# Optimization experiments

Measured on AMD Instinct MI355X. Metric: run time of the kernel, lower is better.

## Reference

```python
import jax, jax.numpy as jnp
import numpy as np

N = 50000      # nodes
E = 800000     # edges (before self-loops)
H = 8          # attention heads
C = 16         # hidden per head (n_hid)
CH = H * C     # 128 = concat channel width
L = 3          # n_layer
F_IN = 128     # n_feat
N_CLASS = 40
NEG_SLOPE = 0.2


def setup_inputs() -> dict:
    key = jax.random.key(0)
    ks = jax.random.split(key, 14)
    s = 0.1
    return {
        "x": jax.random.normal(ks[0], (N, F_IN), jnp.float32),
        "edge_index": jax.random.randint(ks[1], (2, E), 0, N, jnp.int32),
        # layer 0: in F_IN -> H heads of C
        "W0":   jax.random.normal(ks[2], (F_IN, H * C), jnp.float32) * s,
        "as0":  jax.random.normal(ks[3], (H, C), jnp.float32) * s,
        "ad0":  jax.random.normal(ks[4], (H, C), jnp.float32) * s,
        "b0":   jnp.zeros((H * C,), jnp.float32),
        # layers 1..L-1 (stacked): in CH -> H heads of C
        "W12":  jax.random.normal(ks[5], (L - 1, CH, H * C), jnp.float32) * s,
        "as12": jax.random.normal(ks[6], (L - 1, H, C), jnp.float32) * s,
        "ad12": jax.random.normal(ks[7], (L - 1, H, C), jnp.float32) * s,
        "b12":  jnp.zeros((L - 1, H * C), jnp.float32),
        # attention-based skip aggregation over layers
        "Watt": jax.random.normal(ks[8], (CH, CH), jnp.float32) * s,
        "aatt": jax.random.normal(ks[9], (CH,), jnp.float32) * s,
        # output head
        "Wout": jax.random.normal(ks[10], (CH, N_CLASS), jnp.float32) * s,
        "bout": jnp.zeros((N_CLASS,), jnp.float32),
    }


def _gat_layer(x, W, a_src, a_dst, b, src, dst):
    # x: [N, F]; W: [F, H*C]; a_src/a_dst: [H, C]; b: [H*C]
    h = (x @ W).reshape(N, H, C)                                 # [N,H,C]
    s_src = jnp.einsum("nhc,hc->nh", h, a_src)                   # [N,H]
    s_dst = jnp.einsum("nhc,hc->nh", h, a_dst)                   # [N,H]
    e = jax.nn.leaky_relu(s_src[src] + s_dst[dst], NEG_SLOPE)    # [Et,H]
    # segment softmax over incoming edges of each dst node
    e_max = jax.ops.segment_max(e, dst, num_segments=N)          # [N,H]
    ee = jnp.exp(e - e_max[dst])
    denom = jax.ops.segment_sum(ee, dst, num_segments=N)         # [N,H]
    alpha = ee / (denom[dst] + 1e-16)                            # [Et,H]
    msg = h[src] * alpha[:, :, None]                             # [Et,H,C]
    out = jax.ops.segment_sum(msg, dst, num_segments=N)          # [N,H,C]
    return out.reshape(N, H * C) + b


def reference(x, edge_index, W0, as0, ad0, b0, W12, as12, ad12, b12,
              Watt, aatt, Wout, bout):
    src, dst = edge_index[0], edge_index[1]
    loops = jnp.arange(N, dtype=src.dtype)                       # self-loops (PyG default)
    src = jnp.concatenate([src, loops])
    dst = jnp.concatenate([dst, loops])

    h = jax.nn.elu(_gat_layer(x, W0, as0, ad0, b0, src, dst))
    hs = [h]
    for l in range(L - 1):
        h = jax.nn.elu(_gat_layer(h, W12[l], as12[l], ad12[l], b12[l], src, dst))
        hs.append(h)

    hstack = jnp.stack(hs, axis=1)                               # [N,L,CH]
    scores = jnp.einsum("nlc,c->nl", jnp.tanh(jnp.einsum("nlc,cd->nld", hstack, Watt)), aatt)
    lam = jax.nn.softmax(scores, axis=1)                         # [N,L] over layers
    hfinal = jnp.einsum("nlc,nl->nc", hstack, lam)               # [N,CH]
    return hfinal @ Wout + bout
```

## Files before the change

### kernel.cpp

```cpp
#include <hip/hip_runtime.h>
#include <hip/hip_bf16.h>

typedef float f32x4 __attribute__((ext_vector_type(4)));
typedef short bf16x8 __attribute__((ext_vector_type(8)));

#define BCAP 20480

__device__ __forceinline__ float4 ld4(const float* p){ return *reinterpret_cast<const float4*>(p); }
__device__ __forceinline__ unsigned short f2bf(float f){
  unsigned int u = __float_as_uint(f);
  u = (u + 0x7fffu + ((u>>16)&1u)) >> 16;
  return (unsigned short)u;
}
__device__ __forceinline__ float bflo(unsigned int u){ return __uint_as_float(u<<16); }
__device__ __forceinline__ float bfhi(unsigned int u){ return __uint_as_float(u & 0xffff0000u); }
__device__ __forceinline__ float bfs(short s){ return __uint_as_float(((unsigned)(unsigned short)s)<<16); }
__device__ __forceinline__ float ftanh(float x){
  float e = __expf(2.f*x);
  return fmaf(-2.f, __builtin_amdgcn_rcpf(e+1.f), 1.f);
}

__global__ __launch_bounds__(256) void k_bucket(const int* __restrict__ ei, int* __restrict__ bcnt,
                                                unsigned* __restrict__ bdata, int E_, int Et){
  __shared__ int h[64];
  __shared__ int base[64];
  int t = threadIdx.x;
  if (t < 64) h[t] = 0;
  __syncthreads();
  int e0 = blockIdx.x*2048 + t;
  int dv[8], sv[8], rv[8];
  #pragma unroll
  for (int k=0;k<8;k++){
    int e = e0 + k*256;
    if (e < Et){
      int s, d;
      if (e < E_){ s = ei[e]; d = ei[E_+e]; } else { s = e-E_; d = s; }
      dv[k] = d; sv[k] = s;
      rv[k] = atomicAdd(&h[d>>10], 1);
    } else dv[k] = -1;
  }
  __syncthreads();
  if (t < 64 && h[t]) base[t] = atomicAdd(&bcnt[t], h[t]);
  __syncthreads();
  #pragma unroll
  for (int k=0;k<8;k++){
    if (dv[k] >= 0){
      int b = dv[k]>>10;
      bdata[(size_t)b*BCAP + base[b] + rv[k]] = ((unsigned)(dv[k]&1023)<<17) | (unsigned)sv[k];
    }
  }
}

__global__ __launch_bounds__(64) void k_binit(const int* __restrict__ bcnt, int* __restrict__ bbase,
                                              int* __restrict__ off, int N_, int nb){
  int l = threadIdx.x;
  int v = (l < nb) ? bcnt[l] : 0;
  int incl = v;
  #pragma unroll
  for (int d=1; d<64; d<<=1){ int u = __shfl_up(incl, d); if (l>=d) incl += u; }
  if (l < nb) bbase[l] = incl - v;
  if (l == 63) off[N_] = incl;
}

__global__ __launch_bounds__(512) void k_bhist_scan(const unsigned* __restrict__ bdata,
                                                    const int* __restrict__ bcnt,
                                                    const int* __restrict__ bbase,
                                                    int* __restrict__ off, int N_){
  __shared__ int c[1024];
  __shared__ int wsum[8];
  int b = blockIdx.x, t = threadIdx.x;
  for (int i=t;i<1024;i+=512) c[i]=0;
  __syncthreads();
  size_t lo = (size_t)b*BCAP;
  size_t hi = lo + bcnt[b];
  for (size_t i=lo+t; i<hi; i+=512) atomicAdd(&c[bdata[i]>>17], 1);
  __syncthreads();
  int c0 = c[2*t], c1 = c[2*t+1];
  int s = c0 + c1;
  int lane = t&63, w = t>>6;
  int incl = s;
  #pragma unroll
  for (int d=1; d<64; d<<=1){ int u = __shfl_up(incl, d); if (lane>=d) incl += u; }
  if (lane==63) wsum[w] = incl;
  __syncthreads();
  int wpre = 0;
  #pragma unroll
  for (int k=0;k<8;k++) if (k<w) wpre += wsum[k];
  int run = bbase[b] + wpre + incl - s;
  int n = (b<<10) + 2*t;
  if (n   < N_) off[n]   = run;
  if (n+1 < N_) off[n+1] = run + c0;
}

__global__ __launch_bounds__(512) void k_bscatter(const unsigned* __restrict__ bdata,
                                                  const int* __restrict__ bcnt,
                                                  const int* __restrict__ off,
                                                  int* __restrict__ csr, int N_){
  __shared__ int cur[1024];
  int b = blockIdx.x, t = threadIdx.x;
  int n0 = b<<10;
  for (int i=t;i<1024;i+=512){ int n = n0+i; cur[i] = (n < N_) ? off[n] : 0; }
  __syncthreads();
  size_t lo = (size_t)b*BCAP;
  size_t hi = lo + bcnt[b];
  for (size_t i=lo+t; i<hi; i+=512){
    unsigned p = bdata[i];
    int pos = atomicAdd(&cur[p>>17], 1);
    csr[pos] = (int)(p & 0x1FFFFu);
  }
}

__global__ __launch_bounds__(256) void k_prep(const float* __restrict__ W0, const float* __restrict__ W12,
    const float* __restrict__ Watt, const float* __restrict__ as0, const float* __restrict__ ad0,
    const float* __restrict__ as12, const float* __restrict__ ad12,
    const float* __restrict__ Wout, unsigned short* __restrict__ dst){
  int b = blockIdx.x, t = threadIdx.x;
  if (b == 4){
    unsigned short* wo = dst + (size_t)4*18432;
    for (int i=t; i<48*128; i+=256){
      int col = i>>7, k = i&127;
      float v = (col < 40) ? Wout[(size_t)k*40 + col] : 0.f;
      unsigned short hi = f2bf(v);
      float r = v - __uint_as_float(((unsigned)hi)<<16);
      wo[i] = hi;
      wo[48*128 + i] = f2bf(r);
    }
    return;
  }
  __shared__ float Wf[64*128];
  const float* W = (b==0) ? W0 : (b==3 ? Watt : W12 + (size_t)(b-1)*16384);
  unsigned short* out = dst + (size_t)b*18432;
  const float* as_ = (b==0) ? as0 : as12 + (size_t)(b-1)*128;
  const float* ad_ = (b==0) ? ad0 : ad12 + (size_t)(b-1)*128;

  for (int half=0; half<2; half++){
    #pragma unroll
    for (int p=0;p<8;p++){
      int i = p*256 + t;
      *reinterpret_cast<float4*>(&Wf[i*4]) = ld4(&W[(size_t)half*8192 + i*4]);
    }
    __syncthreads();
    {
      int col = t>>1, koff = (t&1)*32;
      #pragma unroll
      for (int j=0;j<4;j++){
        unsigned short tmp[8];
        #pragma unroll
        for (int q=0;q<8;q++) tmp[q] = f2bf(Wf[(koff + j*8 + q)*128 + col]);
        *reinterpret_cast<uint4*>(&out[col*128 + half*64 + koff + j*8]) = *reinterpret_cast<const uint4*>(tmp);
      }
    }
    {
      int ce = t>>4;
      int h  = ce & 7;
      if (b < 3){
        const float* av = (ce < 8) ? (as_ + h*16) : (ad_ + h*16);
        float avr[16];
        #pragma unroll
        for (int c2=0;c2<16;c2++) avr[c2] = av[c2];
        #pragma unroll
        for (int i=0;i<4;i++){
          int kl = (t&15) + i*16;
          float s = 0.f;
          #pragma unroll
          for (int c2=0;c2<16;c2++) s += Wf[kl*128 + h*16 + c2]*avr[c2];
          out[(128+ce)*128 + half*64 + kl] = f2bf(s);
        }
      } else {
        #pragma unroll
        for (int i=0;i<4;i++){
          int kl = (t&15) + i*16;
          out[(128+ce)*128 + half*64 + kl] = 0;
        }
      }
    }
    __syncthreads();
  }
}

template<int AF32>
__global__ __launch_bounds__(256) void k_gemm(
    const void* __restrict__ Ap, const unsigned short* __restrict__ Bt,
    unsigned short* __restrict__ C, float* __restrict__ s_src, float* __restrict__ s_dst, int M)
{
  int t = threadIdx.x, lane = t & 63, w = t >> 6;
  int rA = lane & 15, g = lane >> 4;
  int r0 = blockIdx.x*128 + w*32;
  f32x4 z = {0.f,0.f,0.f,0.f};
  f32x4 acc[2][9];
  #pragma unroll
  for (int mf=0;mf<2;mf++)
    #pragma unroll
    for (int nf=0;nf<9;nf++) acc[mf][nf] = z;

  int rowc0 = min(r0 + rA,      M-1);
  int rowc1 = min(r0 + 16 + rA, M-1);
  #pragma unroll
  for (int ks=0; ks<4; ks++){
    int ko = ks*32 + g*8;
    bf16x8 a0, a1;
    if (AF32){
      const float* Af = (const float*)Ap;
      float4 v0 = ld4(&Af[(size_t)rowc0*128 + ko]);
      float4 v1 = ld4(&Af[(size_t)rowc0*128 + ko + 4]);
      float4 v2 = ld4(&Af[(size_t)rowc1*128 + ko]);
      float4 v3 = ld4(&Af[(size_t)rowc1*128 + ko + 4]);
      a0[0]=(short)f2bf(v0.x); a0[1]=(short)f2bf(v0.y); a0[2]=(short)f2bf(v0.z); a0[3]=(short)f2bf(v0.w);
      a0[4]=(short)f2bf(v1.x); a0[5]=(short)f2bf(v1.y); a0[6]=(short)f2bf(v1.z); a0[7]=(short)f2bf(v1.w);
      a1[0]=(short)f2bf(v2.x); a1[1]=(short)f2bf(v2.y); a1[2]=(short)f2bf(v2.z); a1[3]=(short)f2bf(v2.w);
      a1[4]=(short)f2bf(v3.x); a1[5]=(short)f2bf(v3.y); a1[6]=(short)f2bf(v3.z); a1[7]=(short)f2bf(v3.w);
    } else {
      const unsigned short* A = (const unsigned short*)Ap;
      a0 = *reinterpret_cast<const bf16x8*>(A + (size_t)rowc0*128 + ko);
      a1 = *reinterpret_cast<const bf16x8*>(A + (size_t)rowc1*128 + ko);
    }
    #pragma unroll
    for (int nf=0;nf<9;nf++){
      bf16x8 bf_ = *reinterpret_cast<const bf16x8*>(Bt + (size_t)(nf*16+rA)*128 + ko);
      acc[0][nf] = __builtin_amdgcn_mfma_f32_16x16x32_bf16(a0, bf_, acc[0][nf], 0, 0, 0);
      acc[1][nf] = __builtin_amdgcn_mfma_f32_16x16x32_bf16(a1, bf_, acc[1][nf], 0, 0, 0);
    }
  }

  #pragma unroll
  for (int mf=0;mf<2;mf++){
    #pragma unroll
    for (int r=0;r<4;r++){
      int row = r0 + mf*16 + g*4 + r;
      if (row < M){
        #pragma unroll
        for (int nf=0;nf<8;nf++) C[(size_t)row*128 + nf*16 + rA] = f2bf(acc[mf][nf][r]);
        float sv_ = acc[mf][8][r];
        if (rA < 8) s_src[(size_t)row*8 + rA]     = sv_;
        else        s_dst[(size_t)row*8 + rA - 8] = sv_;
      }
    }
  }
}

__global__ __launch_bounds__(256) void k_aggregate(
    const int* __restrict__ off, const int* __restrict__ csr,
    const unsigned short* __restrict__ htmp, const float* __restrict__ s_src,
    const float* __restrict__ s_dst, const float* __restrict__ bias,
    unsigned short* __restrict__ hout, int N_)
{
  __shared__ float esc[4][640];
  __shared__ int   ssrc[4][80];
  int w = threadIdx.x >> 6;
  int lane = threadIdx.x & 63;
  int n = blockIdx.x*4 + w;
  if (n >= N_) return;
  int base = off[n];
  int deg  = off[n+1] - base;
  int c2 = lane & 15;
  int eo = lane >> 4;
  int myh = c2 >> 1;
  float4 sd0 = ld4(&s_dst[(size_t)n*8]);
  float4 sd1 = ld4(&s_dst[(size_t)n*8+4]);
  float sdv[8] = {sd0.x,sd0.y,sd0.z,sd0.w,sd1.x,sd1.y,sd1.z,sd1.w};
  float acc0=0.f,acc1=0.f,acc2=0.f,acc3=0.f,acc4=0.f,acc5=0.f,acc6=0.f,acc7=0.f;
  float dsum = 0.f;
  const char* hb = (const char*)htmp + (c2<<4);

  ssrc[w][64 + (lane&15)] = 0;
  esc[w][(lane>>3)*80 + 64 + (lane&7)*2]     = 0.f;
  esc[w][(lane>>3)*80 + 64 + (lane&7)*2 + 1] = 0.f;

  for (int cb=0; cb<deg; cb+=64){
    int cdeg = min(64, deg-cb);
    int srcj = 0;
    float ee[8];
    if (lane < cdeg){
      srcj = csr[base+cb+lane];
      float4 a0 = ld4(&s_src[(size_t)srcj*8]);
      float4 a1 = ld4(&s_src[(size_t)srcj*8+4]);
      float sv[8] = {a0.x,a0.y,a0.z,a0.w,a1.x,a1.y,a1.z,a1.w};
      #pragma unroll
      for (int h=0;h<8;h++){
        float v = sv[h] + sdv[h];
        v = v > 0.f ? v : 0.2f*v;
        ee[h] = __expf(v);
      }
    } else {
      #pragma unroll
      for (int h=0;h<8;h++) ee[h] = 0.f;
    }
    ssrc[w][lane] = srcj;
    #pragma unroll
    for (int h=0;h<8;h++) esc[w][h*80 + lane] = ee[h];
    asm volatile("s_waitcnt lgkmcnt(0)" ::: "memory");
    __builtin_amdgcn_sched_barrier(0);

    for (int j=0; j<cdeg; j+=16){
      int e0 = j + eo;
      int e1 = j + 4 + eo;
      int e2 = j + 8 + eo;
      int e3 = j + 12 + eo;
      int s0 = ssrc[w][e0];
      int s1 = ssrc[w][e1];
      int s2 = ssrc[w][e2];
      int s3 = ssrc[w][e3];
      float ev0 = esc[w][myh*80 + e0];
      float ev1 = esc[w][myh*80 + e1];
      float ev2 = esc[w][myh*80 + e2];
      float ev3 = esc[w][myh*80 + e3];
      uint4 u0 = *reinterpret_cast<const uint4*>(hb + ((size_t)(unsigned)s0<<8));
      uint4 u1 = *reinterpret_cast<const uint4*>(hb + ((size_t)(unsigned)s1<<8));
      uint4 u2 = *reinterpret_cast<const uint4*>(hb + ((size_t)(unsigned)s2<<8));
      uint4 u3 = *reinterpret_cast<const uint4*>(hb + ((size_t)(unsigned)s3<<8));
      acc0 = fmaf(ev0, bflo(u0.x), acc0);
      acc1 = fmaf(ev0, bfhi(u0.x), acc1);
      acc2 = fmaf(ev0, bflo(u0.y), acc2);
      acc3 = fmaf(ev0, bfhi(u0.y), acc3);
      acc4 = fmaf(ev0, bflo(u0.z), acc4);
      acc5 = fmaf(ev0, bfhi(u0.z), acc5);
      acc6 = fmaf(ev0, bflo(u0.w), acc6);
      acc7 = fmaf(ev0, bfhi(u0.w), acc7);
      acc0 = fmaf(ev1, bflo(u1.x), acc0);
      acc1 = fmaf(ev1, bfhi(u1.x), acc1);
      acc2 = fmaf(ev1, bflo(u1.y), acc2);
      acc3 = fmaf(ev1, bfhi(u1.y), acc3);
      acc4 = fmaf(ev1, bflo(u1.z), acc4);
      acc5 = fmaf(ev1, bfhi(u1.z), acc5);
      acc6 = fmaf(ev1, bflo(u1.w), acc6);
      acc7 = fmaf(ev1, bfhi(u1.w), acc7);
      acc0 = fmaf(ev2, bflo(u2.x), acc0);
      acc1 = fmaf(ev2, bfhi(u2.x), acc1);
      acc2 = fmaf(ev2, bflo(u2.y), acc2);
      acc3 = fmaf(ev2, bfhi(u2.y), acc3);
      acc4 = fmaf(ev2, bflo(u2.z), acc4);
      acc5 = fmaf(ev2, bfhi(u2.z), acc5);
      acc6 = fmaf(ev2, bflo(u2.w), acc6);
      acc7 = fmaf(ev2, bfhi(u2.w), acc7);
      acc0 = fmaf(ev3, bflo(u3.x), acc0);
      acc1 = fmaf(ev3, bfhi(u3.x), acc1);
      acc2 = fmaf(ev3, bflo(u3.y), acc2);
      acc3 = fmaf(ev3, bfhi(u3.y), acc3);
      acc4 = fmaf(ev3, bflo(u3.z), acc4);
      acc5 = fmaf(ev3, bfhi(u3.z), acc5);
      acc6 = fmaf(ev3, bflo(u3.w), acc6);
      acc7 = fmaf(ev3, bfhi(u3.w), acc7);
      dsum += (ev0 + ev1) + (ev2 + ev3);
    }
  }
  acc0 += __shfl_xor(acc0, 16); acc0 += __shfl_xor(acc0, 32);
  acc1 += __shfl_xor(acc1, 16); acc1 += __shfl_xor(acc1, 32);
  acc2 += __shfl_xor(acc2, 16); acc2 += __shfl_xor(acc2, 32);
  acc3 += __shfl_xor(acc3, 16); acc3 += __shfl_xor(acc3, 32);
  acc4 += __shfl_xor(acc4, 16); acc4 += __shfl_xor(acc4, 32);
  acc5 += __shfl_xor(acc5, 16); acc5 += __shfl_xor(acc5, 32);
  acc6 += __shfl_xor(acc6, 16); acc6 += __shfl_xor(acc6, 32);
  acc7 += __shfl_xor(acc7, 16); acc7 += __shfl_xor(acc7, 32);
  dsum += __shfl_xor(dsum, 16); dsum += __shfl_xor(dsum, 32);

  if (eo == 0){
    float inv = 1.f/(dsum + 1e-16f);
    float4 b0 = ld4(&bias[c2*8]);
    float4 b1 = ld4(&bias[c2*8+4]);
    float o0 = fmaf(acc0, inv, b0.x);
    float o1 = fmaf(acc1, inv, b0.y);
    float o2 = fmaf(acc2, inv, b0.z);
    float o3 = fmaf(acc3, inv, b0.w);
    float o4 = fmaf(acc4, inv, b1.x);
    float o5 = fmaf(acc5, inv, b1.y);
    float o6 = fmaf(acc6, inv, b1.z);
    float o7 = fmaf(acc7, inv, b1.w);
    o0 = o0>0.f ? o0 : (__expf(o0)-1.f);
    o1 = o1>0.f ? o1 : (__expf(o1)-1.f);
    o2 = o2>0.f ? o2 : (__expf(o2)-1.f);
    o3 = o3>0.f ? o3 : (__expf(o3)-1.f);
    o4 = o4>0.f ? o4 : (__expf(o4)-1.f);
    o5 = o5>0.f ? o5 : (__expf(o5)-1.f);
    o6 = o6>0.f ? o6 : (__expf(o6)-1.f);
    o7 = o7>0.f ? o7 : (__expf(o7)-1.f);
    uint4 pk;
    pk.x = (unsigned)f2bf(o0) | ((unsigned)f2bf(o1)<<16);
    pk.y = (unsigned)f2bf(o2) | ((unsigned)f2bf(o3)<<16);
    pk.z = (unsigned)f2bf(o4) | ((unsigned)f2bf(o5)<<16);
    pk.w = (unsigned)f2bf(o6) | ((unsigned)f2bf(o7)<<16);
    *reinterpret_cast<uint4*>(&hout[(size_t)n*128 + c2*8]) = pk;
  }
}

__global__ __launch_bounds__(256) void k_final4(
    const unsigned short* __restrict__ h0, const unsigned short* __restrict__ h1,
    const unsigned short* __restrict__ h2,
    const unsigned short* __restrict__ WattT, const float* __restrict__ aatt,
    const unsigned short* __restrict__ WoutT,
    const float* __restrict__ bout, float* __restrict__ out, int M)
{
  int t = threadIdx.x, lane = t & 63, w = t >> 6;
  int rA = lane & 15, g = lane >> 4;
  int r0 = blockIdx.x*64 + w*16;
  int rowc = min(r0 + rA, M-1);

  float av[8];
  #pragma unroll
  for (int nf=0;nf<8;nf++) av[nf] = aatt[nf*16 + rA];

  bf16x8 a[3][4];
  #pragma unroll
  for (int ks=0;ks<4;ks++){
    int ko = ks*32 + g*8;
    a[0][ks] = *reinterpret_cast<const bf16x8*>(h0 + (size_t)rowc*128 + ko);
    a[1][ks] = *reinterpret_cast<const bf16x8*>(h1 + (size_t)rowc*128 + ko);
    a[2][ks] = *reinterpret_cast<const bf16x8*>(h2 + (size_t)rowc*128 + ko);
  }

  float sc[3][4];
  #pragma unroll
  for (int l=0;l<3;l++)
    #pragma unroll
    for (int r=0;r<4;r++) sc[l][r] = 0.f;

  #pragma unroll
  for (int ch=0; ch<4; ch++){
    f32x4 acc[3][2];
    #pragma unroll
    for (int l=0;l<3;l++){ acc[l][0] = (f32x4){0.f,0.f,0.f,0.f}; acc[l][1] = (f32x4){0.f,0.f,0.f,0.f}; }
    #pragma unroll
    for (int ks=0; ks<4; ks++){
      int ko = ks*32 + g*8;
      bf16x8 b0 = *reinterpret_cast<const bf16x8*>(WattT + (size_t)((ch*2+0)*16+rA)*128 + ko);
      bf16x8 b1 = *reinterpret_cast<const bf16x8*>(WattT + (size_t)((ch*2+1)*16+rA)*128 + ko);
      #pragma unroll
      for (int l=0;l<3;l++){
        acc[l][0] = __builtin_amdgcn_mfma_f32_16x16x32_bf16(a[l][ks], b0, acc[l][0], 0, 0, 0);
        acc[l][1] = __builtin_amdgcn_mfma_f32_16x16x32_bf16(a[l][ks], b1, acc[l][1], 0, 0, 0);
      }
    }
    float w0 = av[ch*2], w1 = av[ch*2+1];
    #pragma unroll
    for (int l=0;l<3;l++)
      #pragma unroll
      for (int r=0;r<4;r++)
        sc[l][r] += ftanh(acc[l][0][r])*w0 + ftanh(acc[l][1][r])*w1;
  }
  #pragma unroll
  for (int l=0;l<3;l++)
    #pragma unroll
    for (int r=0;r<4;r++){
      float s = sc[l][r];
      s += __shfl_xor(s, 1);
      s += __shfl_xor(s, 2);
      s += __shfl_xor(s, 4);
      s += __shfl_xor(s, 8);
      sc[l][r] = s;
    }

  float lam[3][4];
  #pragma unroll
  for (int r=0;r<4;r++){
    float m = fmaxf(sc[0][r], fmaxf(sc[1][r], sc[2][r]));
    float e0 = __expf(sc[0][r]-m), e1 = __expf(sc[1][r]-m), e2 = __expf(sc[2][r]-m);
    float inv = 1.f/(e0+e1+e2);
    lam[0][r]=e0*inv; lam[1][r]=e1*inv; lam[2][r]=e2*inv;
  }
  int rsel = rA & 3;
  int srcLane = ((rA>>2)<<4) | rA;
  float p0 = rsel==0 ? lam[0][0] : rsel==1 ? lam[0][1] : rsel==2 ? lam[0][2] : lam[0][3];
  float p1 = rsel==0 ? lam[1][0] : rsel==1 ? lam[1][1] : rsel==2 ? lam[1][2] : lam[1][3];
  float p2 = rsel==0 ? lam[2][0] : rsel==1 ? lam[2][1] : rsel==2 ? lam[2][2] : lam[2][3];
  float lamA[3];
  lamA[0] = __shfl(p0, srcLane);
  lamA[1] = __shfl(p1, srcLane);
  lamA[2] = __shfl(p2, srcLane);

  f32x4 oacc[3];
  #pragma unroll
  for (int nf=0;nf<3;nf++) oacc[nf] = (f32x4){0.f,0.f,0.f,0.f};
  #pragma unroll
  for (int ks=0;ks<4;ks++){
    int ko = ks*32 + g*8;
    bf16x8 asc[3];
    #pragma unroll
    for (int l=0;l<3;l++){
      #pragma unroll
      for (int i=0;i<8;i++) asc[l][i] = (short)f2bf(bfs(a[l][ks][i]) * lamA[l]);
    }
    #pragma unroll
    for (int nf=0;nf<3;nf++){
      bf16x8 bh = *reinterpret_cast<const bf16x8*>(WoutT + (size_t)(nf*16+rA)*128 + ko);
      bf16x8 bl = *reinterpret_cast<const bf16x8*>(WoutT + 6144 + (size_t)(nf*16+rA)*128 + ko);
      #pragma unroll
      for (int l=0;l<3;l++){
        oacc[nf] = __builtin_amdgcn_mfma_f32_16x16x32_bf16(asc[l], bh, oacc[nf], 0, 0, 0);
        oacc[nf] = __builtin_amdgcn_mfma_f32_16x16x32_bf16(asc[l], bl, oacc[nf], 0, 0, 0);
      }
    }
  }

  #pragma unroll
  for (int nf=0;nf<3;nf++){
    int col = nf*16 + rA;
    float bv = (col < 40) ? bout[col] : 0.f;
    #pragma unroll
    for (int r=0;r<4;r++){
      int row = r0 + g*4 + r;
      if (row < M && col < 40) out[(size_t)row*40 + col] = oacc[nf][r] + bv;
    }
  }
}

extern "C" void kernel_launch(void* const* d_in, const int* in_sizes, int n_in,
                              void* d_out, int out_size, void* d_ws, size_t ws_size,
                              hipStream_t stream)
{
  const float* x    = (const float*)d_in[0];
  const int*   ei   = (const int*)d_in[1];
  const float* W0   = (const float*)d_in[2];
  const float* as0  = (const float*)d_in[3];
  const float* ad0  = (const float*)d_in[4];
  const float* b0   = (const float*)d_in[5];
  const float* W12  = (const float*)d_in[6];
  const float* as12 = (const float*)d_in[7];
  const float* ad12 = (const float*)d_in[8];
  const float* b12  = (const float*)d_in[9];
  const float* Watt = (const float*)d_in[10];
  const float* aatt = (const float*)d_in[11];
  const float* Wout = (const float*)d_in[12];
  const float* bout = (const float*)d_in[13];
  const int N_ = in_sizes[0] / 128;
  const int E_ = in_sizes[1] / 2;
  const int Et = E_ + N_;
  const int nb = (N_ + 1023) >> 10;

  char* p = (char*)d_ws;
  auto carve = [&](size_t bytes)->char*{ char* r = p; p += (bytes + 255) & ~(size_t)255; return r; };
  unsigned short* htmp = (unsigned short*)carve((size_t)N_*128*2);
  unsigned short* h0   = (unsigned short*)carve((size_t)N_*128*2);
  unsigned short* h1   = (unsigned short*)carve((size_t)N_*128*2);
  unsigned short* h2   = (unsigned short*)carve((size_t)N_*128*2);
  unsigned short* wsT  = (unsigned short*)carve((size_t)(5*18432 + 48*128)*2);
  float* ssrc_s  = (float*)carve((size_t)N_*8*4);
  float* sdst_s  = (float*)carve((size_t)N_*8*4);
  int* offv      = (int*)carve((size_t)(N_+1)*4);
  int* bcnt      = (int*)carve((size_t)64*4);
  int* bbase     = (int*)carve((size_t)64*4);
  unsigned* bdata= (unsigned*)carve((size_t)64*BCAP*4);
  int* csr       = (int*)carve((size_t)Et*4);

  k_prep<<<5,256,0,stream>>>(W0, W12, Watt, as0, ad0, as12, ad12, Wout, wsT);

  hipMemsetAsync(bcnt, 0, 64*4, stream);
  int gB = (Et + 2047)/2048;
  k_bucket<<<gB,256,0,stream>>>(ei, bcnt, bdata, E_, Et);
  k_binit<<<1,64,0,stream>>>(bcnt, bbase, offv, N_, nb);
  k_bhist_scan<<<nb,512,0,stream>>>(bdata, bcnt, bbase, offv, N_);
  k_bscatter<<<nb,512,0,stream>>>(bdata, bcnt, offv, csr, N_);

  int gM  = (N_+127)/128;
  int gN4 = (N_+3)/4;
  int gF  = (N_+63)/64;
  unsigned short* hl[3] = {h0,h1,h2};
  for (int l=0;l<3;l++){
    const float* bb = (l==0)? b0 : b12 + (size_t)(l-1)*128;
    const unsigned short* Bt = wsT + (size_t)l*18432;
    if (l==0)
      k_gemm<1><<<gM,256,0,stream>>>((const void*)x, Bt, htmp, ssrc_s, sdst_s, N_);
    else
      k_gemm<0><<<gM,256,0,stream>>>((const void*)hl[l-1], Bt, htmp, ssrc_s, sdst_s, N_);
    k_aggregate<<<gN4,256,0,stream>>>(offv, csr, htmp, ssrc_s, sdst_s, bb, hl[l], N_);
  }
  k_final4<<<gF,256,0,stream>>>(h0, h1, h2, wsT + (size_t)3*18432, aatt,
                                wsT + (size_t)4*18432, bout, (float*)d_out, N_);
}
```

Measured before the change: 262.1 us.

## Process two nodes per wavefront in aggregation and fuse CSR histogram with scatter

```diff
diff --git a/kernel.cpp b/kernel.cpp
--- a/kernel.cpp
+++ b/kernel.cpp
@@ -62,18 +62,18 @@
   if (l == 63) off[N_] = incl;
 }
 
-__global__ __launch_bounds__(512) void k_bhist_scan(const unsigned* __restrict__ bdata,
-                                                    const int* __restrict__ bcnt,
-                                                    const int* __restrict__ bbase,
-                                                    int* __restrict__ off, int N_){
+__global__ __launch_bounds__(512) void k_bfinish(const unsigned* __restrict__ bdata,
+                                                 const int* __restrict__ bcnt,
+                                                 const int* __restrict__ bbase,
+                                                 int* __restrict__ off, int* __restrict__ csr, int N_){
   __shared__ int c[1024];
   __shared__ int wsum[8];
   int b = blockIdx.x, t = threadIdx.x;
+  int cnt = bcnt[b];
+  size_t lo = (size_t)b*BCAP;
   for (int i=t;i<1024;i+=512) c[i]=0;
   __syncthreads();
-  size_t lo = (size_t)b*BCAP;
-  size_t hi = lo + bcnt[b];
-  for (size_t i=lo+t; i<hi; i+=512) atomicAdd(&c[bdata[i]>>17], 1);
+  for (int i=t; i<cnt; i+=512) atomicAdd(&c[bdata[lo+i]>>17], 1);
   __syncthreads();
   int c0 = c[2*t], c1 = c[2*t+1];
   int s = c0 + c1;
@@ -90,22 +90,12 @@
   int n = (b<<10) + 2*t;
   if (n   < N_) off[n]   = run;
   if (n+1 < N_) off[n+1] = run + c0;
-}
-
-__global__ __launch_bounds__(512) void k_bscatter(const unsigned* __restrict__ bdata,
-                                                  const int* __restrict__ bcnt,
-                                                  const int* __restrict__ off,
-                                                  int* __restrict__ csr, int N_){
-  __shared__ int cur[1024];
-  int b = blockIdx.x, t = threadIdx.x;
-  int n0 = b<<10;
-  for (int i=t;i<1024;i+=512){ int n = n0+i; cur[i] = (n < N_) ? off[n] : 0; }
-  __syncthreads();
-  size_t lo = (size_t)b*BCAP;
-  size_t hi = lo + bcnt[b];
-  for (size_t i=lo+t; i<hi; i+=512){
-    unsigned p = bdata[i];
-    int pos = atomicAdd(&cur[p>>17], 1);
+  c[2*t]   = run;
+  c[2*t+1] = run + c0;
+  __syncthreads();
+  for (int i=t; i<cnt; i+=512){
+    unsigned p = bdata[lo+i];
+    int pos = atomicAdd(&c[p>>17], 1);
     csr[pos] = (int)(p & 0x1FFFFu);
   }
 }
@@ -244,34 +234,35 @@
     const float* __restrict__ s_dst, const float* __restrict__ bias,
     unsigned short* __restrict__ hout, int N_)
 {
-  __shared__ float esc[4][640];
-  __shared__ int   ssrc[4][80];
+  __shared__ float esc[4][2][288];
+  __shared__ int   ssrc[4][2][32];
   int w = threadIdx.x >> 6;
   int lane = threadIdx.x & 63;
-  int n = blockIdx.x*4 + w;
-  if (n >= N_) return;
-  int base = off[n];
-  int deg  = off[n+1] - base;
-  int c2 = lane & 15;
-  int eo = lane >> 4;
-  int myh = c2 >> 1;
-  float4 sd0 = ld4(&s_dst[(size_t)n*8]);
-  float4 sd1 = ld4(&s_dst[(size_t)n*8+4]);
-  float sdv[8] = {sd0.x,sd0.y,sd0.z,sd0.w,sd1.x,sd1.y,sd1.z,sd1.w};
+  int half = lane >> 5;
+  int l32  = lane & 31;
+  int c2   = l32 & 15;
+  int eo   = l32 >> 4;
+  int myh  = c2 >> 1;
+  int n = blockIdx.x*8 + w*2 + half;
+  int base = 0, deg = 0;
+  if (n < N_){ base = off[n]; deg = off[n+1] - base; }
+  float sdv[8] = {0.f,0.f,0.f,0.f,0.f,0.f,0.f,0.f};
+  if (n < N_){
+    float4 sd0 = ld4(&s_dst[(size_t)n*8]);
+    float4 sd1 = ld4(&s_dst[(size_t)n*8+4]);
+    sdv[0]=sd0.x; sdv[1]=sd0.y; sdv[2]=sd0.z; sdv[3]=sd0.w;
+    sdv[4]=sd1.x; sdv[5]=sd1.y; sdv[6]=sd1.z; sdv[7]=sd1.w;
+  }
   float acc0=0.f,acc1=0.f,acc2=0.f,acc3=0.f,acc4=0.f,acc5=0.f,acc6=0.f,acc7=0.f;
   float dsum = 0.f;
   const char* hb = (const char*)htmp + (c2<<4);
 
-  ssrc[w][64 + (lane&15)] = 0;
-  esc[w][(lane>>3)*80 + 64 + (lane&7)*2]     = 0.f;
-  esc[w][(lane>>3)*80 + 64 + (lane&7)*2 + 1] = 0.f;
-
-  for (int cb=0; cb<deg; cb+=64){
-    int cdeg = min(64, deg-cb);
+  for (int cb=0; cb<deg; cb+=32){
+    int cdeg = min(32, deg-cb);
     int srcj = 0;
     float ee[8];
-    if (lane < cdeg){
-      srcj = csr[base+cb+lane];
+    if (l32 < cdeg){
+      srcj = csr[base+cb+l32];
       float4 a0 = ld4(&s_src[(size_t)srcj*8]);
       float4 a1 = ld4(&s_src[(size_t)srcj*8+4]);
       float sv[8] = {a0.x,a0.y,a0.z,a0.w,a1.x,a1.y,a1.z,a1.w};
@@ -285,29 +276,21 @@
       #pragma unroll
       for (int h=0;h<8;h++) ee[h] = 0.f;
     }
-    ssrc[w][lane] = srcj;
-    #pragma unroll
-    for (int h=0;h<8;h++) esc[w][h*80 + lane] = ee[h];
+    ssrc[w][half][l32] = srcj;
+    #pragma unroll
+    for (int h=0;h<8;h++) esc[w][half][h*36 + l32] = ee[h];
     asm volatile("s_waitcnt lgkmcnt(0)" ::: "memory");
     __builtin_amdgcn_sched_barrier(0);
 
-    for (int j=0; j<cdeg; j+=16){
+    for (int j=0; j<cdeg; j+=4){
       int e0 = j + eo;
-      int e1 = j + 4 + eo;
-      int e2 = j + 8 + eo;
-      int e3 = j + 12 + eo;
-      int s0 = ssrc[w][e0];
-      int s1 = ssrc[w][e1];
-      int s2 = ssrc[w][e2];
-      int s3 = ssrc[w][e3];
-      float ev0 = esc[w][myh*80 + e0];
-      float ev1 = esc[w][myh*80 + e1];
-      float ev2 = esc[w][myh*80 + e2];
-      float ev3 = esc[w][myh*80 + e3];
+      int e1 = j + 2 + eo;
+      int s0 = ssrc[w][half][e0];
+      int s1 = ssrc[w][half][e1];
+      float ev0 = esc[w][half][myh*36 + e0];
+      float ev1 = esc[w][half][myh*36 + e1];
       uint4 u0 = *reinterpret_cast<const uint4*>(hb + ((size_t)(unsigned)s0<<8));
       uint4 u1 = *reinterpret_cast<const uint4*>(hb + ((size_t)(unsigned)s1<<8));
-      uint4 u2 = *reinterpret_cast<const uint4*>(hb + ((size_t)(unsigned)s2<<8));
-      uint4 u3 = *reinterpret_cast<const uint4*>(hb + ((size_t)(unsigned)s3<<8));
       acc0 = fmaf(ev0, bflo(u0.x), acc0);
       acc1 = fmaf(ev0, bfhi(u0.x), acc1);
       acc2 = fmaf(ev0, bflo(u0.y), acc2);
@@ -324,36 +307,20 @@
       acc5 = fmaf(ev1, bfhi(u1.z), acc5);
       acc6 = fmaf(ev1, bflo(u1.w), acc6);
       acc7 = fmaf(ev1, bfhi(u1.w), acc7);
-      acc0 = fmaf(ev2, bflo(u2.x), acc0);
-      acc1 = fmaf(ev2, bfhi(u2.x), acc1);
-      acc2 = fmaf(ev2, bflo(u2.y), acc2);
-      acc3 = fmaf(ev2, bfhi(u2.y), acc3);
-      acc4 = fmaf(ev2, bflo(u2.z), acc4);
-      acc5 = fmaf(ev2, bfhi(u2.z), acc5);
-      acc6 = fmaf(ev2, bflo(u2.w), acc6);
-      acc7 = fmaf(ev2, bfhi(u2.w), acc7);
-      acc0 = fmaf(ev3, bflo(u3.x), acc0);
-      acc1 = fmaf(ev3, bfhi(u3.x), acc1);
-      acc2 = fmaf(ev3, bflo(u3.y), acc2);
-      acc3 = fmaf(ev3, bfhi(u3.y), acc3);
-      acc4 = fmaf(ev3, bflo(u3.z), acc4);
-      acc5 = fmaf(ev3, bfhi(u3.z), acc5);
-      acc6 = fmaf(ev3, bflo(u3.w), acc6);
-      acc7 = fmaf(ev3, bfhi(u3.w), acc7);
-      dsum += (ev0 + ev1) + (ev2 + ev3);
-    }
-  }
-  acc0 += __shfl_xor(acc0, 16); acc0 += __shfl_xor(acc0, 32);
-  acc1 += __shfl_xor(acc1, 16); acc1 += __shfl_xor(acc1, 32);
-  acc2 += __shfl_xor(acc2, 16); acc2 += __shfl_xor(acc2, 32);
-  acc3 += __shfl_xor(acc3, 16); acc3 += __shfl_xor(acc3, 32);
-  acc4 += __shfl_xor(acc4, 16); acc4 += __shfl_xor(acc4, 32);
-  acc5 += __shfl_xor(acc5, 16); acc5 += __shfl_xor(acc5, 32);
-  acc6 += __shfl_xor(acc6, 16); acc6 += __shfl_xor(acc6, 32);
-  acc7 += __shfl_xor(acc7, 16); acc7 += __shfl_xor(acc7, 32);
-  dsum += __shfl_xor(dsum, 16); dsum += __shfl_xor(dsum, 32);
-
-  if (eo == 0){
+      dsum += ev0 + ev1;
+    }
+  }
+  acc0 += __shfl_xor(acc0, 16);
+  acc1 += __shfl_xor(acc1, 16);
+  acc2 += __shfl_xor(acc2, 16);
+  acc3 += __shfl_xor(acc3, 16);
+  acc4 += __shfl_xor(acc4, 16);
+  acc5 += __shfl_xor(acc5, 16);
+  acc6 += __shfl_xor(acc6, 16);
+  acc7 += __shfl_xor(acc7, 16);
+  dsum += __shfl_xor(dsum, 16);
+
+  if (n < N_ && eo == 0){
     float inv = 1.f/(dsum + 1e-16f);
     float4 b0 = ld4(&bias[c2*8]);
     float4 b1 = ld4(&bias[c2*8+4]);
@@ -546,11 +513,10 @@
   int gB = (Et + 2047)/2048;
   k_bucket<<<gB,256,0,stream>>>(ei, bcnt, bdata, E_, Et);
   k_binit<<<1,64,0,stream>>>(bcnt, bbase, offv, N_, nb);
-  k_bhist_scan<<<nb,512,0,stream>>>(bdata, bcnt, bbase, offv, N_);
-  k_bscatter<<<nb,512,0,stream>>>(bdata, bcnt, offv, csr, N_);
+  k_bfinish<<<nb,512,0,stream>>>(bdata, bcnt, bbase, offv, csr, N_);
 
   int gM  = (N_+127)/128;
-  int gN4 = (N_+3)/4;
+  int gN8 = (N_+7)/8;
   int gF  = (N_+63)/64;
   unsigned short* hl[3] = {h0,h1,h2};
   for (int l=0;l<3;l++){
@@ -560,7 +526,7 @@
       k_gemm<1><<<gM,256,0,stream>>>((const void*)x, Bt, htmp, ssrc_s, sdst_s, N_);
     else
       k_gemm<0><<<gM,256,0,stream>>>((const void*)hl[l-1], Bt, htmp, ssrc_s, sdst_s, N_);
-    k_aggregate<<<gN4,256,0,stream>>>(offv, csr, htmp, ssrc_s, sdst_s, bb, hl[l], N_);
+    k_aggregate<<<gN8,256,0,stream>>>(offv, csr, htmp, ssrc_s, sdst_s, bb, hl[l], N_);
   }
   k_final4<<<gF,256,0,stream>>>(h0, h1, h2, wsT + (size_t)3*18432, aatt,
                                 wsT + (size_t)4*18432, bout, (float*)d_out, N_);
```

Result: faster. 246.9 us (-5.8%).
